# Kernel tuning notes

Hardware: AMD Instinct MI355X
Metric: run time of the kernel (lower is better)

The kernel has to match this reference:

```python
import jax, jax.numpy as jnp
import numpy as np

N, OBS, H, M, L = 512, 32, 128, 128, 3


def _w(key, shape, fan_in):
    return jax.random.normal(key, shape, dtype=jnp.float32) / np.sqrt(fan_in)


def setup_inputs() -> dict:
    key = jax.random.key(0)
    ks = iter(jax.random.split(key, 64))
    inp = {}
    inp["obs"] = jax.random.normal(next(ks), (N, OBS), dtype=jnp.float32)
    inp["pos"] = jax.random.uniform(next(ks), (N, 2), dtype=jnp.float32)
    # encoder: obs_dim -> H -> H -> H
    inp["enc_W1"] = _w(next(ks), (H, OBS), OBS); inp["enc_b1"] = jnp.zeros((H,), jnp.float32)
    inp["enc_W2"] = _w(next(ks), (H, H), H);     inp["enc_b2"] = jnp.zeros((H,), jnp.float32)
    inp["enc_W3"] = _w(next(ks), (H, H), H);     inp["enc_b3"] = jnp.zeros((H,), jnp.float32)
    # per-layer message MLPs: (2H+1) -> M -> M -> M, stacked over L layers
    inp["msg_W1"] = _w(next(ks), (L, M, 2 * H + 1), 2 * H + 1); inp["msg_b1"] = jnp.zeros((L, M), jnp.float32)
    inp["msg_W2"] = _w(next(ks), (L, M, M), M);                 inp["msg_b2"] = jnp.zeros((L, M), jnp.float32)
    inp["msg_W3"] = _w(next(ks), (L, M, M), M);                 inp["msg_b3"] = jnp.zeros((L, M), jnp.float32)
    # per-layer update MLPs: (H+M) -> H -> H -> H, stacked over L layers
    inp["upd_W1"] = _w(next(ks), (L, H, H + M), H + M); inp["upd_b1"] = jnp.zeros((L, H), jnp.float32)
    inp["upd_W2"] = _w(next(ks), (L, H, H), H);         inp["upd_b2"] = jnp.zeros((L, H), jnp.float32)
    inp["upd_W3"] = _w(next(ks), (L, H, H), H);         inp["upd_b3"] = jnp.zeros((L, H), jnp.float32)
    return inp


def _mlp3(x, W1, b1, W2, b2, W3, b3):
    h = jax.nn.relu(x @ W1.T + b1)
    h = jax.nn.relu(h @ W2.T + b2)
    return h @ W3.T + b3


def reference(obs, pos, enc_W1, enc_b1, enc_W2, enc_b2, enc_W3, enc_b3,
              msg_W1, msg_b1, msg_W2, msg_b2, msg_W3, msg_b3,
              upd_W1, upd_b1, upd_W2, upd_b2, upd_W3, upd_b3):
    n = obs.shape[0]
    h = enc_W1.shape[0]
    z = _mlp3(obs, enc_W1, enc_b1, enc_W2, enc_b2, enc_W3, enc_b3)  # (N, H)
    # pairwise distances; guard diagonal sqrt(0) for grad safety, then zero it
    diff = pos[:, None, :] - pos[None, :, :]                  # (N, N, 2)
    sq = jnp.sum(diff * diff, axis=-1)                        # (N, N)
    eye = jnp.eye(n, dtype=pos.dtype)
    dist = jnp.sqrt(jnp.where(eye > 0, 1.0, sq)) * (1.0 - eye)
    nondiag = (1.0 - eye)[:, :, None]
    n_layers = msg_W1.shape[0]
    for l in range(n_layers):
        W1 = msg_W1[l]
        Wi, Wj, wd = W1[:, :h], W1[:, h:2 * h], W1[:, 2 * h]  # split concat [z_i, z_j, d]
        A = z @ Wi.T                                          # (N, M) receiver term
        B = z @ Wj.T                                          # (N, M) sender term
        h1 = jax.nn.relu(A[:, None, :] + B[None, :, :] + dist[:, :, None] * wd + msg_b1[l])  # (N, N, M)
        h2 = jax.nn.relu(jnp.einsum('ijm,km->ijk', h1, msg_W2[l]) + msg_b2[l])
        m = jnp.einsum('ijm,km->ijk', h2, msg_W3[l]) + msg_b3[l]
        m = m * nondiag                                       # exclude j == i
        msum = jnp.sum(m, axis=1)                             # (N, M) sum over senders j
        z = _mlp3(jnp.concatenate([z, msum], axis=-1),
                  upd_W1[l], upd_b1[l], upd_W2[l], upd_b2[l], upd_W3[l], upd_b3[l])
    return z
```

## Files before the change

kernel.cpp:

```cpp
#include <hip/hip_runtime.h>

#define NA 512
#define NOBS 32
#define NH 128

typedef const float* fp32p;
typedef __attribute__((ext_vector_type(8))) short bf16x8;
typedef __attribute__((ext_vector_type(4))) float f32x4;

__device__ __forceinline__ short f2bf(float f) {
    union { float f; unsigned u; } v; v.f = f;
    unsigned r = v.u + 0x7fffu + ((v.u >> 16) & 1u);
    return (short)(r >> 16);
}

__device__ __forceinline__ bf16x8 wfrag_f4(const float* p) {
    float4 u = *(const float4*)p;
    float4 v = *(const float4*)(p + 4);
    bf16x8 f;
    f[0] = f2bf(u.x); f[1] = f2bf(u.y); f[2] = f2bf(u.z); f[3] = f2bf(u.w);
    f[4] = f2bf(v.x); f[5] = f2bf(v.y); f[6] = f2bf(v.z); f[7] = f2bf(v.w);
    return f;
}
__device__ __forceinline__ bf16x8 wfrag_s(const float* p) {
    bf16x8 f;
    #pragma unroll
    for (int j = 0; j < 8; ++j) f[j] = f2bf(p[j]);
    return f;
}

#define HSTR 136
#define XSTR 40
#define USTR 264

__global__ __launch_bounds__(512) void enc_ab_kernel(
    fp32p obs, fp32p W1, fp32p b1, fp32p W2, fp32p b2, fp32p W3, fp32p b3,
    fp32p msgW1, float* __restrict__ z, float* __restrict__ A, float* __restrict__ B) {
    const int a0 = blockIdx.x * 64;
    const int t = threadIdx.x;
    const int lane = t & 63, w = t >> 6, q = lane >> 4, c = lane & 15;
    const int ncol = w * 16 + c;

    __shared__ short xs[64 * XSTR];
    __shared__ short h1s[64 * HSTR];
    __shared__ short h2s[64 * HSTR];

    for (int e = t; e < 64 * NOBS; e += 512) {
        int r = e >> 5, k = e & 31;
        xs[r * XSTR + k] = f2bf(obs[(size_t)(a0 + r) * NOBS + k]);
    }
    bf16x8 wf = wfrag_f4(W1 + (size_t)ncol * NOBS + q * 8);
    const float bias1 = b1[ncol];
    __syncthreads();
    #pragma unroll
    for (int jt = 0; jt < 4; ++jt) {
        f32x4 acc = {0.f, 0.f, 0.f, 0.f};
        bf16x8 a = *(const bf16x8*)&xs[(jt * 16 + c) * XSTR + q * 8];
        acc = __builtin_amdgcn_mfma_f32_16x16x32_bf16(a, wf, acc, 0, 0, 0);
        #pragma unroll
        for (int r = 0; r < 4; ++r)
            h1s[(jt * 16 + q * 4 + r) * HSTR + ncol] = f2bf(fmaxf(acc[r] + bias1, 0.f));
    }
    bf16x8 w2f[4];
    #pragma unroll
    for (int kb = 0; kb < 4; ++kb) w2f[kb] = wfrag_f4(W2 + (size_t)ncol * NH + kb * 32 + q * 8);
    const float bias2 = b2[ncol];
    __syncthreads();
    #pragma unroll
    for (int jt = 0; jt < 4; ++jt) {
        f32x4 acc = {0.f, 0.f, 0.f, 0.f};
        #pragma unroll
        for (int kb = 0; kb < 4; ++kb) {
            bf16x8 a = *(const bf16x8*)&h1s[(jt * 16 + c) * HSTR + kb * 32 + q * 8];
            acc = __builtin_amdgcn_mfma_f32_16x16x32_bf16(a, w2f[kb], acc, 0, 0, 0);
        }
        #pragma unroll
        for (int r = 0; r < 4; ++r)
            h2s[(jt * 16 + q * 4 + r) * HSTR + ncol] = f2bf(fmaxf(acc[r] + bias2, 0.f));
    }
    bf16x8 w3f[4];
    #pragma unroll
    for (int kb = 0; kb < 4; ++kb) w3f[kb] = wfrag_f4(W3 + (size_t)ncol * NH + kb * 32 + q * 8);
    const float bias3 = b3[ncol];
    __syncthreads();
    #pragma unroll
    for (int jt = 0; jt < 4; ++jt) {
        f32x4 acc = {0.f, 0.f, 0.f, 0.f};
        #pragma unroll
        for (int kb = 0; kb < 4; ++kb) {
            bf16x8 a = *(const bf16x8*)&h2s[(jt * 16 + c) * HSTR + kb * 32 + q * 8];
            acc = __builtin_amdgcn_mfma_f32_16x16x32_bf16(a, w3f[kb], acc, 0, 0, 0);
        }
        #pragma unroll
        for (int r = 0; r < 4; ++r) {
            const int row = jt * 16 + q * 4 + r;
            const float v = acc[r] + bias3;
            z[(size_t)(a0 + row) * NH + ncol] = v;
            h1s[row * HSTR + ncol] = f2bf(v);
        }
    }
    bf16x8 wif[4], wjf[4];
    #pragma unroll
    for (int kb = 0; kb < 4; ++kb) {
        const float* pr = msgW1 + (size_t)ncol * 257 + kb * 32 + q * 8;
        wif[kb] = wfrag_s(pr);
        wjf[kb] = wfrag_s(pr + NH);
    }
    __syncthreads();
    #pragma unroll
    for (int jt = 0; jt < 4; ++jt) {
        f32x4 accA = {0.f, 0.f, 0.f, 0.f};
        f32x4 accB = {0.f, 0.f, 0.f, 0.f};
        #pragma unroll
        for (int kb = 0; kb < 4; ++kb) {
            bf16x8 a = *(const bf16x8*)&h1s[(jt * 16 + c) * HSTR + kb * 32 + q * 8];
            accA = __builtin_amdgcn_mfma_f32_16x16x32_bf16(a, wif[kb], accA, 0, 0, 0);
            accB = __builtin_amdgcn_mfma_f32_16x16x32_bf16(a, wjf[kb], accB, 0, 0, 0);
        }
        #pragma unroll
        for (int r = 0; r < 4; ++r) {
            const int row = jt * 16 + q * 4 + r;
            A[(size_t)(a0 + row) * NH + ncol] = accA[r];
            B[(size_t)(a0 + row) * NH + ncol] = accB[r];
        }
    }
}

__global__ __launch_bounds__(512) void msg_kernel(
    const float* __restrict__ A, const float* __restrict__ B,
    fp32p pos,
    fp32p W1l, fp32p b1, fp32p W2, fp32p b2, fp32p W3, fp32p b3,
    float* __restrict__ msum) {
    const int i = blockIdx.x;
    const int t = threadIdx.x;
    const int lane = t & 63;
    const int w = t >> 6;
    const int q = lane >> 4;
    const int c = lane & 15;
    const int ncol = w * 16 + c;

    __shared__ short h1s[64 * HSTR];
    __shared__ short h2s[64 * HSTR];
    __shared__ float distrow[NA];
    __shared__ float amrow[NH];
    __shared__ float wdsr[NH];

    if (t < NH) {
        amrow[t] = A[i * NH + t] + b1[t];
        wdsr[t]  = W1l[t * 257 + 256];
    }
    {
        const float2 pi = *(const float2*)&pos[2 * i];
        const float2 pj = *(const float2*)&pos[2 * t];
        const float dx = pi.x - pj.x, dy = pi.y - pj.y;
        const float s = dx * dx + dy * dy;
        distrow[t] = (t == i) ? 0.0f : sqrtf(s);
    }

    bf16x8 w2f[4], w3f[4];
    {
        const float* w2r = W2 + (size_t)ncol * NH + q * 8;
        const float* w3r = W3 + (size_t)ncol * NH + q * 8;
        #pragma unroll
        for (int kb = 0; kb < 4; ++kb) {
            w2f[kb] = wfrag_f4(w2r + kb * 32);
            w3f[kb] = wfrag_f4(w3r + kb * 32);
        }
    }
    const float b2n = b2[ncol];
    const float b3n = b3[ncol];

    const int m2 = lane * 2;
    float psum = 0.0f;

    for (int c8 = 0; c8 < 8; ++c8) {
        const int j0 = c8 * 64;
        __syncthreads();

        {
            const float am0 = amrow[m2],     am1 = amrow[m2 + 1];
            const float wd0 = wdsr[m2],      wd1 = wdsr[m2 + 1];
            #pragma unroll
            for (int rr = 0; rr < 8; ++rr) {
                const int row = rr * 8 + w;
                const int jg  = j0 + row;
                const float2 bv = *(const float2*)&B[(size_t)jg * NH + m2];
                const float d = distrow[jg];
                const float v0 = fmaxf(am0 + bv.x + d * wd0, 0.0f);
                const float v1 = fmaxf(am1 + bv.y + d * wd1, 0.0f);
                const unsigned p = (unsigned)(unsigned short)f2bf(v0) |
                                   ((unsigned)(unsigned short)f2bf(v1) << 16);
                *(unsigned*)&h1s[row * HSTR + m2] = p;
            }
        }
        __syncthreads();

        #pragma unroll
        for (int jt = 0; jt < 4; ++jt) {
            f32x4 acc = {0.f, 0.f, 0.f, 0.f};
            const short* arow = &h1s[(jt * 16 + c) * HSTR + q * 8];
            #pragma unroll
            for (int kb = 0; kb < 4; ++kb) {
                bf16x8 a = *(const bf16x8*)(arow + kb * 32);
                acc = __builtin_amdgcn_mfma_f32_16x16x32_bf16(a, w2f[kb], acc, 0, 0, 0);
            }
            #pragma unroll
            for (int r = 0; r < 4; ++r) {
                const int row = jt * 16 + q * 4 + r;
                h2s[row * HSTR + ncol] = f2bf(fmaxf(acc[r] + b2n, 0.0f));
            }
        }
        __syncthreads();

        #pragma unroll
        for (int jt = 0; jt < 4; ++jt) {
            f32x4 acc = {0.f, 0.f, 0.f, 0.f};
            const short* arow = &h2s[(jt * 16 + c) * HSTR + q * 8];
            #pragma unroll
            for (int kb = 0; kb < 4; ++kb) {
                bf16x8 a = *(const bf16x8*)(arow + kb * 32);
                acc = __builtin_amdgcn_mfma_f32_16x16x32_bf16(a, w3f[kb], acc, 0, 0, 0);
            }
            #pragma unroll
            for (int r = 0; r < 4; ++r) {
                const int jg = j0 + jt * 16 + q * 4 + r;
                if (jg != i) psum += acc[r] + b3n;
            }
        }
    }

    psum += __shfl_xor(psum, 16, 64);
    psum += __shfl_xor(psum, 32, 64);
    if (lane < 16) msum[i * NH + ncol] = psum;
}

__global__ __launch_bounds__(512) void upd_ab_kernel(
    fp32p zin, fp32p ms,
    fp32p W1, fp32p b1, fp32p W2, fp32p b2, fp32p W3, fp32p b3,
    fp32p msgW1n, int do_ab,
    float* __restrict__ zout, float* __restrict__ A, float* __restrict__ B) {
    const int a0 = blockIdx.x * 64;
    const int t = threadIdx.x;
    const int lane = t & 63, w = t >> 6, q = lane >> 4, c = lane & 15;
    const int ncol = w * 16 + c;

    __shared__ short xs[64 * USTR];
    __shared__ short h1s[64 * HSTR];
    __shared__ short h2s[64 * HSTR];

    for (int e = t; e < 64 * 256; e += 512) {
        int r = e >> 8, k = e & 255;
        float v = (k < NH) ? zin[(size_t)(a0 + r) * NH + k]
                           : ms[(size_t)(a0 + r) * NH + (k - NH)];
        xs[r * USTR + k] = f2bf(v);
    }
    bf16x8 w1f[8];
    #pragma unroll
    for (int kb = 0; kb < 8; ++kb) w1f[kb] = wfrag_f4(W1 + (size_t)ncol * 256 + kb * 32 + q * 8);
    const float bias1 = b1[ncol];
    __syncthreads();
    #pragma unroll
    for (int jt = 0; jt < 4; ++jt) {
        f32x4 acc = {0.f, 0.f, 0.f, 0.f};
        #pragma unroll
        for (int kb = 0; kb < 8; ++kb) {
            bf16x8 a = *(const bf16x8*)&xs[(jt * 16 + c) * USTR + kb * 32 + q * 8];
            acc = __builtin_amdgcn_mfma_f32_16x16x32_bf16(a, w1f[kb], acc, 0, 0, 0);
        }
        #pragma unroll
        for (int r = 0; r < 4; ++r)
            h1s[(jt * 16 + q * 4 + r) * HSTR + ncol] = f2bf(fmaxf(acc[r] + bias1, 0.f));
    }
    bf16x8 w2f[4];
    #pragma unroll
    for (int kb = 0; kb < 4; ++kb) w2f[kb] = wfrag_f4(W2 + (size_t)ncol * NH + kb * 32 + q * 8);
    const float bias2 = b2[ncol];
    __syncthreads();
    #pragma unroll
    for (int jt = 0; jt < 4; ++jt) {
        f32x4 acc = {0.f, 0.f, 0.f, 0.f};
        #pragma unroll
        for (int kb = 0; kb < 4; ++kb) {
            bf16x8 a = *(const bf16x8*)&h1s[(jt * 16 + c) * HSTR + kb * 32 + q * 8];
            acc = __builtin_amdgcn_mfma_f32_16x16x32_bf16(a, w2f[kb], acc, 0, 0, 0);
        }
        #pragma unroll
        for (int r = 0; r < 4; ++r)
            h2s[(jt * 16 + q * 4 + r) * HSTR + ncol] = f2bf(fmaxf(acc[r] + bias2, 0.f));
    }
    bf16x8 w3f[4];
    #pragma unroll
    for (int kb = 0; kb < 4; ++kb) w3f[kb] = wfrag_f4(W3 + (size_t)ncol * NH + kb * 32 + q * 8);
    const float bias3 = b3[ncol];
    __syncthreads();
    #pragma unroll
    for (int jt = 0; jt < 4; ++jt) {
        f32x4 acc = {0.f, 0.f, 0.f, 0.f};
        #pragma unroll
        for (int kb = 0; kb < 4; ++kb) {
            bf16x8 a = *(const bf16x8*)&h2s[(jt * 16 + c) * HSTR + kb * 32 + q * 8];
            acc = __builtin_amdgcn_mfma_f32_16x16x32_bf16(a, w3f[kb], acc, 0, 0, 0);
        }
        #pragma unroll
        for (int r = 0; r < 4; ++r) {
            const int row = jt * 16 + q * 4 + r;
            const float v = acc[r] + bias3;
            zout[(size_t)(a0 + row) * NH + ncol] = v;
            if (do_ab) h1s[row * HSTR + ncol] = f2bf(v);
        }
    }
    if (!do_ab) return;
    bf16x8 wif[4], wjf[4];
    #pragma unroll
    for (int kb = 0; kb < 4; ++kb) {
        const float* pr = msgW1n + (size_t)ncol * 257 + kb * 32 + q * 8;
        wif[kb] = wfrag_s(pr);
        wjf[kb] = wfrag_s(pr + NH);
    }
    __syncthreads();
    #pragma unroll
    for (int jt = 0; jt < 4; ++jt) {
        f32x4 accA = {0.f, 0.f, 0.f, 0.f};
        f32x4 accB = {0.f, 0.f, 0.f, 0.f};
        #pragma unroll
        for (int kb = 0; kb < 4; ++kb) {
            bf16x8 a = *(const bf16x8*)&h1s[(jt * 16 + c) * HSTR + kb * 32 + q * 8];
            accA = __builtin_amdgcn_mfma_f32_16x16x32_bf16(a, wif[kb], accA, 0, 0, 0);
            accB = __builtin_amdgcn_mfma_f32_16x16x32_bf16(a, wjf[kb], accB, 0, 0, 0);
        }
        #pragma unroll
        for (int r = 0; r < 4; ++r) {
            const int row = jt * 16 + q * 4 + r;
            A[(size_t)(a0 + row) * NH + ncol] = accA[r];
            B[(size_t)(a0 + row) * NH + ncol] = accB[r];
        }
    }
}

extern "C" void kernel_launch(void* const* d_in, const int* in_sizes, int n_in,
                              void* d_out, int out_size, void* d_ws, size_t ws_size,
                              hipStream_t stream) {
    fp32p obs   = (fp32p)d_in[0];
    fp32p pos   = (fp32p)d_in[1];
    fp32p encW1 = (fp32p)d_in[2];  fp32p encb1 = (fp32p)d_in[3];
    fp32p encW2 = (fp32p)d_in[4];  fp32p encb2 = (fp32p)d_in[5];
    fp32p encW3 = (fp32p)d_in[6];  fp32p encb3 = (fp32p)d_in[7];
    fp32p msgW1 = (fp32p)d_in[8];  fp32p msgb1 = (fp32p)d_in[9];
    fp32p msgW2 = (fp32p)d_in[10]; fp32p msgb2 = (fp32p)d_in[11];
    fp32p msgW3 = (fp32p)d_in[12]; fp32p msgb3 = (fp32p)d_in[13];
    fp32p updW1 = (fp32p)d_in[14]; fp32p updb1 = (fp32p)d_in[15];
    fp32p updW2 = (fp32p)d_in[16]; fp32p updb2 = (fp32p)d_in[17];
    fp32p updW3 = (fp32p)d_in[18]; fp32p updb3 = (fp32p)d_in[19];

    float* ws = (float*)d_ws;
    float* zA = ws;
    float* zB = zA + NA * NH;
    float* Ab = zB + NA * NH;
    float* Bb = Ab + NA * NH;
    float* ms = Bb + NA * NH;

    enc_ab_kernel<<<8, 512, 0, stream>>>(obs, encW1, encb1, encW2, encb2,
                                         encW3, encb3, msgW1, zA, Ab, Bb);

    float* zin = zA;
    float* zout = zB;
    for (int l = 0; l < 3; ++l) {
        msg_kernel<<<NA, 512, 0, stream>>>(Ab, Bb, pos,
            msgW1 + (size_t)l * 128 * 257, msgb1 + l * 128,
            msgW2 + (size_t)l * 128 * 128, msgb2 + l * 128,
            msgW3 + (size_t)l * 128 * 128, msgb3 + l * 128, ms);
        const int do_ab = (l < 2);
        float* dst = (l == 2) ? (float*)d_out : zout;
        upd_ab_kernel<<<8, 512, 0, stream>>>(zin, ms,
            updW1 + (size_t)l * 256 * 128, updb1 + l * 128,
            updW2 + (size_t)l * 128 * 128, updb2 + l * 128,
            updW3 + (size_t)l * 128 * 128, updb3 + l * 128,
            msgW1 + (size_t)(l + 1) * 128 * 257, do_ab, dst, Ab, Bb);
        float* tmp = zin; zin = zout; zout = tmp;
    }
}
```

Measured before the change: 256.0 us.

## Fuse update MLP and next-layer A/B projection into message kernel

Each message block now finishes its own row: it keeps the message sum in shared memory, then runs the per-node update MLP and the next layer's A/B projections with fp32 scalar dot products split across four thread groups. This removes the separate 8-block update kernel and its launch, plus the global round-trip of msum. A and B are double-buffered so reads of the current layer's values don't race with writes of the next. The encoder is also retiled to 16 rows per block with 32 blocks to spread it over more CUs. The trade-off is that each of the 512 message blocks now re-reads all update weights with non-MFMA fp32 math.

```diff
diff --git a/kernel.cpp b/kernel.cpp
--- a/kernel.cpp
+++ b/kernel.cpp
@@ -31,69 +31,65 @@
 
 #define HSTR 136
 #define XSTR 40
-#define USTR 264
 
 __global__ __launch_bounds__(512) void enc_ab_kernel(
     fp32p obs, fp32p W1, fp32p b1, fp32p W2, fp32p b2, fp32p W3, fp32p b3,
     fp32p msgW1, float* __restrict__ z, float* __restrict__ A, float* __restrict__ B) {
-    const int a0 = blockIdx.x * 64;
+    const int a0 = blockIdx.x * 16;
     const int t = threadIdx.x;
     const int lane = t & 63, w = t >> 6, q = lane >> 4, c = lane & 15;
     const int ncol = w * 16 + c;
 
-    __shared__ short xs[64 * XSTR];
-    __shared__ short h1s[64 * HSTR];
-    __shared__ short h2s[64 * HSTR];
-
-    for (int e = t; e < 64 * NOBS; e += 512) {
-        int r = e >> 5, k = e & 31;
+    __shared__ short xs[16 * XSTR];
+    __shared__ short h1s[16 * HSTR];
+    __shared__ short h2s[16 * HSTR];
+
+    {
+        const int r = t >> 5, k = t & 31;
         xs[r * XSTR + k] = f2bf(obs[(size_t)(a0 + r) * NOBS + k]);
     }
     bf16x8 wf = wfrag_f4(W1 + (size_t)ncol * NOBS + q * 8);
     const float bias1 = b1[ncol];
     __syncthreads();
-    #pragma unroll
-    for (int jt = 0; jt < 4; ++jt) {
+    {
         f32x4 acc = {0.f, 0.f, 0.f, 0.f};
-        bf16x8 a = *(const bf16x8*)&xs[(jt * 16 + c) * XSTR + q * 8];
+        bf16x8 a = *(const bf16x8*)&xs[c * XSTR + q * 8];
         acc = __builtin_amdgcn_mfma_f32_16x16x32_bf16(a, wf, acc, 0, 0, 0);
         #pragma unroll
         for (int r = 0; r < 4; ++r)
-            h1s[(jt * 16 + q * 4 + r) * HSTR + ncol] = f2bf(fmaxf(acc[r] + bias1, 0.f));
+            h1s[(q * 4 + r) * HSTR + ncol] = f2bf(fmaxf(acc[r] + bias1, 0.f));
     }
     bf16x8 w2f[4];
     #pragma unroll
     for (int kb = 0; kb < 4; ++kb) w2f[kb] = wfrag_f4(W2 + (size_t)ncol * NH + kb * 32 + q * 8);
     const float bias2 = b2[ncol];
     __syncthreads();
-    #pragma unroll
-    for (int jt = 0; jt < 4; ++jt) {
+    {
         f32x4 acc = {0.f, 0.f, 0.f, 0.f};
         #pragma unroll
         for (int kb = 0; kb < 4; ++kb) {
-            bf16x8 a = *(const bf16x8*)&h1s[(jt * 16 + c) * HSTR + kb * 32 + q * 8];
+            bf16x8 a = *(const bf16x8*)&h1s[c * HSTR + kb * 32 + q * 8];
             acc = __builtin_amdgcn_mfma_f32_16x16x32_bf16(a, w2f[kb], acc, 0, 0, 0);
         }
         #pragma unroll
         for (int r = 0; r < 4; ++r)
-            h2s[(jt * 16 + q * 4 + r) * HSTR + ncol] = f2bf(fmaxf(acc[r] + bias2, 0.f));
+            h2s[(q * 4 + r) * HSTR + ncol] = f2bf(fmaxf(acc[r] + bias2, 0.f));
     }
     bf16x8 w3f[4];
     #pragma unroll
     for (int kb = 0; kb < 4; ++kb) w3f[kb] = wfrag_f4(W3 + (size_t)ncol * NH + kb * 32 + q * 8);
     const float bias3 = b3[ncol];
     __syncthreads();
-    #pragma unroll
-    for (int jt = 0; jt < 4; ++jt) {
+    {
         f32x4 acc = {0.f, 0.f, 0.f, 0.f};
         #pragma unroll
         for (int kb = 0; kb < 4; ++kb) {
-            bf16x8 a = *(const bf16x8*)&h2s[(jt * 16 + c) * HSTR + kb * 32 + q * 8];
+            bf16x8 a = *(const bf16x8*)&h2s[c * HSTR + kb * 32 + q * 8];
             acc = __builtin_amdgcn_mfma_f32_16x16x32_bf16(a, w3f[kb], acc, 0, 0, 0);
         }
         #pragma unroll
         for (int r = 0; r < 4; ++r) {
-            const int row = jt * 16 + q * 4 + r;
+            const int row = q * 4 + r;
             const float v = acc[r] + bias3;
             z[(size_t)(a0 + row) * NH + ncol] = v;
             h1s[row * HSTR + ncol] = f2bf(v);
@@ -107,30 +103,31 @@
         wjf[kb] = wfrag_s(pr + NH);
     }
     __syncthreads();
-    #pragma unroll
-    for (int jt = 0; jt < 4; ++jt) {
+    {
         f32x4 accA = {0.f, 0.f, 0.f, 0.f};
         f32x4 accB = {0.f, 0.f, 0.f, 0.f};
         #pragma unroll
         for (int kb = 0; kb < 4; ++kb) {
-            bf16x8 a = *(const bf16x8*)&h1s[(jt * 16 + c) * HSTR + kb * 32 + q * 8];
+            bf16x8 a = *(const bf16x8*)&h1s[c * HSTR + kb * 32 + q * 8];
             accA = __builtin_amdgcn_mfma_f32_16x16x32_bf16(a, wif[kb], accA, 0, 0, 0);
             accB = __builtin_amdgcn_mfma_f32_16x16x32_bf16(a, wjf[kb], accB, 0, 0, 0);
         }
         #pragma unroll
         for (int r = 0; r < 4; ++r) {
-            const int row = jt * 16 + q * 4 + r;
+            const int row = q * 4 + r;
             A[(size_t)(a0 + row) * NH + ncol] = accA[r];
             B[(size_t)(a0 + row) * NH + ncol] = accB[r];
         }
     }
 }
 
-__global__ __launch_bounds__(512) void msg_kernel(
+__global__ __launch_bounds__(512) void msg_upd_kernel(
     const float* __restrict__ A, const float* __restrict__ B,
-    fp32p pos,
+    fp32p pos, const float* __restrict__ zin,
     fp32p W1l, fp32p b1, fp32p W2, fp32p b2, fp32p W3, fp32p b3,
-    float* __restrict__ msum) {
+    fp32p uW1, fp32p ub1, fp32p uW2, fp32p ub2, fp32p uW3, fp32p ub3,
+    fp32p msgW1n, int do_ab,
+    float* __restrict__ zout, float* __restrict__ An, float* __restrict__ Bn) {
     const int i = blockIdx.x;
     const int t = threadIdx.x;
     const int lane = t & 63;
@@ -144,6 +141,10 @@
     __shared__ float distrow[NA];
     __shared__ float amrow[NH];
     __shared__ float wdsr[NH];
+    __shared__ float msum_s[NH];
+    __shared__ float xs2[2 * NH];
+    __shared__ float part[4 * NH * 2];
+    __shared__ float hx[NH], hy[NH];
 
     if (t < NH) {
         amrow[t] = A[i * NH + t] + b1[t];
@@ -231,109 +232,83 @@
 
     psum += __shfl_xor(psum, 16, 64);
     psum += __shfl_xor(psum, 32, 64);
-    if (lane < 16) msum[i * NH + ncol] = psum;
-}
-
-__global__ __launch_bounds__(512) void upd_ab_kernel(
-    fp32p zin, fp32p ms,
-    fp32p W1, fp32p b1, fp32p W2, fp32p b2, fp32p W3, fp32p b3,
-    fp32p msgW1n, int do_ab,
-    float* __restrict__ zout, float* __restrict__ A, float* __restrict__ B) {
-    const int a0 = blockIdx.x * 64;
-    const int t = threadIdx.x;
-    const int lane = t & 63, w = t >> 6, q = lane >> 4, c = lane & 15;
-    const int ncol = w * 16 + c;
-
-    __shared__ short xs[64 * USTR];
-    __shared__ short h1s[64 * HSTR];
-    __shared__ short h2s[64 * HSTR];
-
-    for (int e = t; e < 64 * 256; e += 512) {
-        int r = e >> 8, k = e & 255;
-        float v = (k < NH) ? zin[(size_t)(a0 + r) * NH + k]
-                           : ms[(size_t)(a0 + r) * NH + (k - NH)];
-        xs[r * USTR + k] = f2bf(v);
-    }
-    bf16x8 w1f[8];
-    #pragma unroll
-    for (int kb = 0; kb < 8; ++kb) w1f[kb] = wfrag_f4(W1 + (size_t)ncol * 256 + kb * 32 + q * 8);
-    const float bias1 = b1[ncol];
-    __syncthreads();
-    #pragma unroll
-    for (int jt = 0; jt < 4; ++jt) {
-        f32x4 acc = {0.f, 0.f, 0.f, 0.f};
-        #pragma unroll
-        for (int kb = 0; kb < 8; ++kb) {
-            bf16x8 a = *(const bf16x8*)&xs[(jt * 16 + c) * USTR + kb * 32 + q * 8];
-            acc = __builtin_amdgcn_mfma_f32_16x16x32_bf16(a, w1f[kb], acc, 0, 0, 0);
-        }
-        #pragma unroll
-        for (int r = 0; r < 4; ++r)
-            h1s[(jt * 16 + q * 4 + r) * HSTR + ncol] = f2bf(fmaxf(acc[r] + bias1, 0.f));
-    }
-    bf16x8 w2f[4];
-    #pragma unroll
-    for (int kb = 0; kb < 4; ++kb) w2f[kb] = wfrag_f4(W2 + (size_t)ncol * NH + kb * 32 + q * 8);
-    const float bias2 = b2[ncol];
-    __syncthreads();
-    #pragma unroll
-    for (int jt = 0; jt < 4; ++jt) {
-        f32x4 acc = {0.f, 0.f, 0.f, 0.f};
-        #pragma unroll
-        for (int kb = 0; kb < 4; ++kb) {
-            bf16x8 a = *(const bf16x8*)&h1s[(jt * 16 + c) * HSTR + kb * 32 + q * 8];
-            acc = __builtin_amdgcn_mfma_f32_16x16x32_bf16(a, w2f[kb], acc, 0, 0, 0);
-        }
-        #pragma unroll
-        for (int r = 0; r < 4; ++r)
-            h2s[(jt * 16 + q * 4 + r) * HSTR + ncol] = f2bf(fmaxf(acc[r] + bias2, 0.f));
-    }
-    bf16x8 w3f[4];
-    #pragma unroll
-    for (int kb = 0; kb < 4; ++kb) w3f[kb] = wfrag_f4(W3 + (size_t)ncol * NH + kb * 32 + q * 8);
-    const float bias3 = b3[ncol];
-    __syncthreads();
-    #pragma unroll
-    for (int jt = 0; jt < 4; ++jt) {
-        f32x4 acc = {0.f, 0.f, 0.f, 0.f};
-        #pragma unroll
-        for (int kb = 0; kb < 4; ++kb) {
-            bf16x8 a = *(const bf16x8*)&h2s[(jt * 16 + c) * HSTR + kb * 32 + q * 8];
-            acc = __builtin_amdgcn_mfma_f32_16x16x32_bf16(a, w3f[kb], acc, 0, 0, 0);
-        }
-        #pragma unroll
-        for (int r = 0; r < 4; ++r) {
-            const int row = jt * 16 + q * 4 + r;
-            const float v = acc[r] + bias3;
-            zout[(size_t)(a0 + row) * NH + ncol] = v;
-            if (do_ab) h1s[row * HSTR + ncol] = f2bf(v);
-        }
+    if (lane < 16) msum_s[ncol] = psum;
+    __syncthreads();
+
+    const int n = t & 127;
+    const int s = t >> 7;
+    if (t < NH)            xs2[t] = zin[(size_t)i * NH + t];
+    else if (t < 2 * NH)   xs2[t] = msum_s[t - NH];
+    __syncthreads();
+    {
+        const float* wr = uW1 + (size_t)n * 256 + s * 64;
+        const float* xr = xs2 + s * 64;
+        float p = 0.f;
+        #pragma unroll
+        for (int kk = 0; kk < 64; kk += 4) {
+            float4 wv = *(const float4*)(wr + kk);
+            float4 xv = *(const float4*)(xr + kk);
+            p += wv.x * xv.x + wv.y * xv.y + wv.z * xv.z + wv.w * xv.w;
+        }
+        part[s * NH + n] = p;
+    }
+    __syncthreads();
+    if (t < NH)
+        hx[t] = fmaxf(ub1[t] + part[t] + part[NH + t] + part[2 * NH + t] + part[3 * NH + t], 0.f);
+    __syncthreads();
+    {
+        const float* wr = uW2 + (size_t)n * NH + s * 32;
+        const float* xr = hx + s * 32;
+        float p = 0.f;
+        #pragma unroll
+        for (int kk = 0; kk < 32; kk += 4) {
+            float4 wv = *(const float4*)(wr + kk);
+            float4 xv = *(const float4*)(xr + kk);
+            p += wv.x * xv.x + wv.y * xv.y + wv.z * xv.z + wv.w * xv.w;
+        }
+        part[s * NH + n] = p;
+    }
+    __syncthreads();
+    if (t < NH)
+        hy[t] = fmaxf(ub2[t] + part[t] + part[NH + t] + part[2 * NH + t] + part[3 * NH + t], 0.f);
+    __syncthreads();
+    {
+        const float* wr = uW3 + (size_t)n * NH + s * 32;
+        const float* xr = hy + s * 32;
+        float p = 0.f;
+        #pragma unroll
+        for (int kk = 0; kk < 32; kk += 4) {
+            float4 wv = *(const float4*)(wr + kk);
+            float4 xv = *(const float4*)(xr + kk);
+            p += wv.x * xv.x + wv.y * xv.y + wv.z * xv.z + wv.w * xv.w;
+        }
+        part[s * NH + n] = p;
+    }
+    __syncthreads();
+    if (t < NH) {
+        const float v = ub3[t] + part[t] + part[NH + t] + part[2 * NH + t] + part[3 * NH + t];
+        zout[(size_t)i * NH + t] = v;
+        hx[t] = v;
     }
     if (!do_ab) return;
-    bf16x8 wif[4], wjf[4];
-    #pragma unroll
-    for (int kb = 0; kb < 4; ++kb) {
-        const float* pr = msgW1n + (size_t)ncol * 257 + kb * 32 + q * 8;
-        wif[kb] = wfrag_s(pr);
-        wjf[kb] = wfrag_s(pr + NH);
-    }
-    __syncthreads();
-    #pragma unroll
-    for (int jt = 0; jt < 4; ++jt) {
-        f32x4 accA = {0.f, 0.f, 0.f, 0.f};
-        f32x4 accB = {0.f, 0.f, 0.f, 0.f};
-        #pragma unroll
-        for (int kb = 0; kb < 4; ++kb) {
-            bf16x8 a = *(const bf16x8*)&h1s[(jt * 16 + c) * HSTR + kb * 32 + q * 8];
-            accA = __builtin_amdgcn_mfma_f32_16x16x32_bf16(a, wif[kb], accA, 0, 0, 0);
-            accB = __builtin_amdgcn_mfma_f32_16x16x32_bf16(a, wjf[kb], accB, 0, 0, 0);
-        }
-        #pragma unroll
-        for (int r = 0; r < 4; ++r) {
-            const int row = jt * 16 + q * 4 + r;
-            A[(size_t)(a0 + row) * NH + ncol] = accA[r];
-            B[(size_t)(a0 + row) * NH + ncol] = accB[r];
-        }
+    __syncthreads();
+    {
+        const float* wr = msgW1n + (size_t)n * 257 + s * 32;
+        const float* xr = hx + s * 32;
+        float pa = 0.f, pb = 0.f;
+        #pragma unroll
+        for (int kk = 0; kk < 32; ++kk) {
+            const float x = xr[kk];
+            pa += x * wr[kk];
+            pb += x * wr[NH + kk];
+        }
+        part[s * NH + n] = pa;
+        part[4 * NH + s * NH + n] = pb;
+    }
+    __syncthreads();
+    if (t < NH) {
+        An[(size_t)i * NH + t] = part[t] + part[NH + t] + part[2 * NH + t] + part[3 * NH + t];
+        Bn[(size_t)i * NH + t] = part[4 * NH + t] + part[5 * NH + t] + part[6 * NH + t] + part[7 * NH + t];
     }
 }
 
@@ -355,27 +330,32 @@
     float* ws = (float*)d_ws;
     float* zA = ws;
     float* zB = zA + NA * NH;
-    float* Ab = zB + NA * NH;
-    float* Bb = Ab + NA * NH;
-    float* ms = Bb + NA * NH;
-
-    enc_ab_kernel<<<8, 512, 0, stream>>>(obs, encW1, encb1, encW2, encb2,
-                                         encW3, encb3, msgW1, zA, Ab, Bb);
-
-    float* zin = zA;
-    float* zout = zB;
+    float* A0 = zB + NA * NH;
+    float* B0 = A0 + NA * NH;
+    float* A1 = B0 + NA * NH;
+    float* B1 = A1 + NA * NH;
+
+    enc_ab_kernel<<<32, 512, 0, stream>>>(obs, encW1, encb1, encW2, encb2,
+                                          encW3, encb3, msgW1, zA, A0, B0);
+
+    float* zin = zA;  float* zout = zB;
+    float* Ac = A0;   float* Bc = B0;
+    float* An = A1;   float* Bn = B1;
     for (int l = 0; l < 3; ++l) {
-        msg_kernel<<<NA, 512, 0, stream>>>(Ab, Bb, pos,
+        const int do_ab = (l < 2);
+        float* dst = (l == 2) ? (float*)d_out : zout;
+        msg_upd_kernel<<<NA, 512, 0, stream>>>(Ac, Bc, pos, zin,
             msgW1 + (size_t)l * 128 * 257, msgb1 + l * 128,
             msgW2 + (size_t)l * 128 * 128, msgb2 + l * 128,
-            msgW3 + (size_t)l * 128 * 128, msgb3 + l * 128, ms);
-        const int do_ab = (l < 2);
-        float* dst = (l == 2) ? (float*)d_out : zout;
-        upd_ab_kernel<<<8, 512, 0, stream>>>(zin, ms,
+            msgW3 + (size_t)l * 128 * 128, msgb3 + l * 128,
             updW1 + (size_t)l * 256 * 128, updb1 + l * 128,
             updW2 + (size_t)l * 128 * 128, updb2 + l * 128,
             updW3 + (size_t)l * 128 * 128, updb3 + l * 128,
-            msgW1 + (size_t)(l + 1) * 128 * 257, do_ab, dst, Ab, Bb);
-        float* tmp = zin; zin = zout; zout = tmp;
-    }
-}
+            msgW1 + (size_t)(l + 1 < 3 ? l + 1 : 0) * 128 * 257, do_ab,
+            dst, An, Bn);
+        float* tmp;
+        tmp = zin; zin = zout; zout = tmp;
+        tmp = Ac; Ac = An; An = tmp;
+        tmp = Bc; Bc = Bn; Bn = tmp;
+    }
+}
```

Result: slower. 261.9 us (+2.3%).
